# Kernel optimization log

Hardware: AMD Instinct MI355X
Metric: run time of the kernel (lower is better)

## Reference

```python
import jax, jax.numpy as jnp
import numpy as np

N = 100000
E = 1600000
IN_DIM = 128
OUT_DIM = 128
NEG_SLOPE = 0.01  # F.leaky_relu default


def setup_inputs() -> dict:
    key = jax.random.key(0)
    k1, k2, k3, k4, k5, k6 = jax.random.split(key, 6)
    feat = jax.random.normal(k1, (N, IN_DIM), dtype=jnp.float32)
    biclique_mask = jax.random.uniform(k2, (IN_DIM,), dtype=jnp.float32)
    W = jax.random.normal(k3, (OUT_DIM, IN_DIM), dtype=jnp.float32) * 0.05
    attn = jax.random.normal(k4, (OUT_DIM,), dtype=jnp.float32) * 0.1
    src = jax.random.randint(k5, (E,), 0, N, dtype=jnp.int32)
    dst = jax.random.randint(k6, (E,), 0, N, dtype=jnp.int32)
    return {"feat": feat, "biclique_mask": biclique_mask, "W": W,
            "attn": attn, "src": src, "dst": dst}


def reference(feat, biclique_mask, W, attn, src, dst):
    # h = Linear(feat * mask), no bias
    h = (feat * biclique_mask[None, :]) @ W.T            # [N, out_dim]
    # edge score depends only on src node -> compute per-node then gather
    s = jax.nn.leaky_relu(h @ attn, negative_slope=NEG_SLOPE)  # [N]
    score = s[src]                                        # [E]
    # edge softmax grouped by destination node
    seg_max = jax.ops.segment_max(score, dst, num_segments=N)  # [N]
    seg_max = jnp.where(jnp.isfinite(seg_max), seg_max, 0.0)   # empty segs
    ex = jnp.exp(score - seg_max[dst])                     # [E]
    denom = jax.ops.segment_sum(ex, dst, num_segments=N)   # [N]
    a = ex / denom[dst]                                    # [E]
    # weighted aggregation: sum_{e: dst(e)=v} h[src(e)] * a[e]
    m = h[src] * a[:, None]                                # [E, out_dim]
    h_new = jax.ops.segment_sum(m, dst, num_segments=N)    # [N, out_dim]
    return jax.nn.relu(h_new)
```

## Files before the change

### kernel.cpp

```cpp
#include <hip/hip_runtime.h>
#include <math.h>

#define NN 100000
#define EE 1600000
#define DIM 128

#define BK 512
#define NBK2 196
#define NCH 256
#define EPB 6250
#define SCN (NBK2 * NCH)
#define NSB 49

typedef _Float16 half8 __attribute__((ext_vector_type(8)));
typedef _Float16 half2v __attribute__((ext_vector_type(2)));
typedef float f32x4 __attribute__((ext_vector_type(4)));

__global__ __launch_bounds__(256) void k_wt(const float* __restrict__ W,
                                            const float* __restrict__ mask,
                                            _Float16* __restrict__ Bt) {
    int o = blockIdx.x * 256 + threadIdx.x;
    if (o < DIM * DIM) Bt[o] = (_Float16)(W[o] * mask[o & 127]);
}

__global__ __launch_bounds__(256) void k_gemm(const float* __restrict__ feat,
                                              const _Float16* __restrict__ Bt,
                                              const float* __restrict__ attn,
                                              _Float16* __restrict__ hh,
                                              float* __restrict__ s) {
    const int lane = threadIdx.x & 63;
    const int wv   = threadIdx.x >> 6;
    const int l15  = lane & 15;
    const int quad = lane >> 4;
    const int row0 = blockIdx.x * 64 + wv * 16;

    f32x4 acc[8];
#pragma unroll
    for (int nt = 0; nt < 8; ++nt) acc[nt] = (f32x4){0.f, 0.f, 0.f, 0.f};

    const int arow = row0 + l15;
    const bool okA = arow < NN;
    const float* ap = feat + (size_t)(okA ? arow : 0) * DIM + quad * 8;

#pragma unroll
    for (int kc = 0; kc < 4; ++kc) {
        half8 a;
        float4 f0 = ((const float4*)(ap + kc * 32))[0];
        float4 f1 = ((const float4*)(ap + kc * 32))[1];
        if (!okA) { f0 = make_float4(0, 0, 0, 0); f1 = make_float4(0, 0, 0, 0); }
        a[0] = (_Float16)f0.x; a[1] = (_Float16)f0.y;
        a[2] = (_Float16)f0.z; a[3] = (_Float16)f0.w;
        a[4] = (_Float16)f1.x; a[5] = (_Float16)f1.y;
        a[6] = (_Float16)f1.z; a[7] = (_Float16)f1.w;
#pragma unroll
        for (int nt = 0; nt < 8; ++nt) {
            half8 b = *(const half8*)(Bt + (size_t)(nt * 16 + l15) * DIM + kc * 32 + quad * 8);
            acc[nt] = __builtin_amdgcn_mfma_f32_16x16x32_f16(a, b, acc[nt], 0, 0, 0);
        }
    }

    float avv[8];
#pragma unroll
    for (int nt = 0; nt < 8; ++nt) avv[nt] = attn[nt * 16 + l15];

#pragma unroll
    for (int r = 0; r < 4; ++r) {
        int row = row0 + quad * 4 + r;
        float p = 0.f;
#pragma unroll
        for (int nt = 0; nt < 8; ++nt) p += acc[nt][r] * avv[nt];
        p += __shfl_xor(p, 1, 64);
        p += __shfl_xor(p, 2, 64);
        p += __shfl_xor(p, 4, 64);
        p += __shfl_xor(p, 8, 64);
        if (l15 == 0 && row < NN) {
            float lr = (p > 0.f) ? p : 0.01f * p;
            s[row] = __expf(lr);
        }
    }

#pragma unroll
    for (int nt = 0; nt < 8; ++nt) {
#pragma unroll
        for (int r = 0; r < 4; ++r) {
            int row = row0 + quad * 4 + r;
            if (row < NN)
                hh[(size_t)row * DIM + nt * 16 + l15] = (_Float16)acc[nt][r];
        }
    }
}

__global__ __launch_bounds__(1024) void k_bhist(const int* __restrict__ dst,
                                                int* __restrict__ gHist) {
    __shared__ int hist[NBK2];
    const int t = threadIdx.x, b = blockIdx.x;
    for (int i = t; i < NBK2; i += 1024) hist[i] = 0;
    __syncthreads();
    const int e0 = b * EPB;
    int e1 = e0 + EPB; if (e1 > EE) e1 = EE;
    for (int e = e0 + t; e < e1; e += 1024)
        atomicAdd(&hist[dst[e] >> 9], 1);
    __syncthreads();
    for (int i = t; i < NBK2; i += 1024)
        gHist[i * NCH + b] = hist[i];
}

__global__ __launch_bounds__(256) void k_scan_a(const int* __restrict__ deg,
                                                int* __restrict__ excl,
                                                int* __restrict__ bsum) {
    __shared__ int wsum[4];
    __shared__ int woff[4];
    const int t = threadIdx.x, b = blockIdx.x;
    const int base = b * 1024 + t * 4;
    int v0 = deg[base + 0];
    int v1 = deg[base + 1];
    int v2 = deg[base + 2];
    int v3 = deg[base + 3];
    int tsum = v0 + v1 + v2 + v3;

    const int lane = t & 63, w = t >> 6;
    int incl = tsum;
#pragma unroll
    for (int d = 1; d < 64; d <<= 1) {
        int n = __shfl_up(incl, d, 64);
        if (lane >= d) incl += n;
    }
    if (lane == 63) wsum[w] = incl;
    __syncthreads();
    if (t == 0) {
        int run = 0;
#pragma unroll
        for (int i = 0; i < 4; ++i) { woff[i] = run; run += wsum[i]; }
        bsum[b] = run;
    }
    __syncthreads();
    int texcl = incl - tsum + woff[w];
    excl[base + 0] = texcl;
    excl[base + 1] = texcl + v0;
    excl[base + 2] = texcl + v0 + v1;
    excl[base + 3] = texcl + v0 + v1 + v2;
}

__global__ __launch_bounds__(64) void k_scan_b(const int* __restrict__ bsum,
                                               int* __restrict__ boff) {
    const int lane = threadIdx.x & 63;
    int v = (lane < NSB) ? bsum[lane] : 0;
    int incl = v;
#pragma unroll
    for (int d = 1; d < 64; d <<= 1) {
        int n = __shfl_up(incl, d, 64);
        if (lane >= d) incl += n;
    }
    if (lane < NSB) boff[lane] = incl - v;
}

__global__ __launch_bounds__(1024) void k_bscatter(const int* __restrict__ src,
                                                   const int* __restrict__ dst,
                                                   const float* __restrict__ s,
                                                   const int* __restrict__ gOff,
                                                   const int* __restrict__ boff,
                                                   int2* __restrict__ binned) {
    __shared__ int cur[NBK2];
    const int t = threadIdx.x, b = blockIdx.x;
    for (int i = t; i < NBK2; i += 1024) {
        int idx = i * NCH + b;
        cur[i] = gOff[idx] + boff[idx >> 10];
    }
    __syncthreads();
    const int e0 = b * EPB;
    int e1 = e0 + EPB; if (e1 > EE) e1 = EE;
    for (int e = e0 + t; e < e1; e += 1024) {
        int d  = dst[e];
        int si = src[e];
        float x = s[si];
        int bk   = d >> 9;
        int dloc = d & (BK - 1);
        int pos = atomicAdd(&cur[bk], 1);
        binned[pos] = make_int2(si | (dloc << 20), __float_as_int(x));
    }
}

__global__ __launch_bounds__(1024) void k_group(const int* __restrict__ gOff,
                                                const int* __restrict__ boff,
                                                const int2* __restrict__ binned,
                                                int2* __restrict__ pack,
                                                int* __restrict__ offs) {
    __shared__ int ldeg[BK];
    __shared__ int wpart[8];
    const int bk = blockIdx.x;
    const int t  = threadIdx.x;
    const int i0 = bk * NCH;
    const int base = gOff[i0] + boff[i0 >> 10];
    int endp;
    if (bk == NBK2 - 1) endp = EE;
    else {
        int i1 = (bk + 1) * NCH;
        endp = gOff[i1] + boff[i1 >> 10];
    }

    if (t < BK) ldeg[t] = 0;
    __syncthreads();
    for (int j = base + t; j < endp; j += 1024)
        atomicAdd(&ldeg[(binned[j].x >> 20) & (BK - 1)], 1);
    __syncthreads();

    int v = 0, incl = 0;
    const int lane = t & 63;
    if (t < BK) {
        v = ldeg[t];
        incl = v;
#pragma unroll
        for (int d = 1; d < 64; d <<= 1) {
            int n = __shfl_up(incl, d, 64);
            if (lane >= d) incl += n;
        }
        if (lane == 63) wpart[t >> 6] = incl;
    }
    __syncthreads();
    if (t == 0) {
        int run = 0;
#pragma unroll
        for (int i = 0; i < 8; ++i) { int tmp = wpart[i]; wpart[i] = run; run += tmp; }
    }
    __syncthreads();
    if (t < BK) {
        int excl = incl - v + wpart[t >> 6];
        int c = base + excl;
        int n = bk * BK + t;
        if (n < NN) offs[n] = c;
        ldeg[t] = c;
    }
    if (bk == NBK2 - 1 && t == 0) offs[NN] = EE;
    __syncthreads();

    for (int j = base + t; j < endp; j += 1024) {
        int2 e = binned[j];
        int dloc = (e.x >> 20) & (BK - 1);
        int si   = e.x & 0xFFFFF;
        int pos = atomicAdd(&ldeg[dloc], 1);
        pack[pos] = make_int2(si, e.y);
    }
}

__global__ __launch_bounds__(256) void k_agg(const _Float16* __restrict__ hh,
                                             const int* __restrict__ offs,
                                             const int2* __restrict__ pack,
                                             float* __restrict__ out) {
    const int lane = threadIdx.x & 63;
    const int g    = lane >> 4;
    const int li   = lane & 15;
    const int wid  = __builtin_amdgcn_readfirstlane(blockIdx.x * 4 + (threadIdx.x >> 6));
    if (wid >= NN) return;
    const int beg = __builtin_amdgcn_readfirstlane(offs[wid]);
    const int end = __builtin_amdgcn_readfirstlane(offs[wid + 1]);
    const int deg = end - beg;

    const half8* h8 = (const half8*)hh;
    float acc[8];
#pragma unroll
    for (int k = 0; k < 8; ++k) acc[k] = 0.f;
    float lsum = 0.f;

    for (int base = 0; base < deg; base += 64) {
        const int nrem = deg - base;
        const int idx  = base + lane;
        const int cl   = (idx < deg) ? idx : (deg - 1);
        const int2 e   = pack[beg + cl];
        const float w  = (idx < deg) ? __int_as_float(e.y) : 0.f;
        lsum += w;
        const int cmax = (nrem < 64) ? nrem : 64;
        for (int c0 = 0; c0 < cmax; c0 += 16) {
#pragma unroll
            for (int s = 0; s < 4; ++s) {
                const int ei = c0 + s * 4 + g;
                const int   si = __shfl(e.x, ei, 64);
                const float wg = __shfl(w,   ei, 64);
                half8 v = h8[((unsigned)si << 4) + li];
#pragma unroll
                for (int k = 0; k < 8; ++k)
                    acc[k] = fmaf((float)v[k], wg, acc[k]);
            }
        }
    }

#pragma unroll
    for (int k = 0; k < 8; ++k) {
        acc[k] += __shfl_xor(acc[k], 16, 64);
        acc[k] += __shfl_xor(acc[k], 32, 64);
    }
    lsum += __shfl_xor(lsum, 1, 64);
    lsum += __shfl_xor(lsum, 2, 64);
    lsum += __shfl_xor(lsum, 4, 64);
    lsum += __shfl_xor(lsum, 8, 64);
    lsum += __shfl_xor(lsum, 16, 64);
    lsum += __shfl_xor(lsum, 32, 64);

    const float inv = (lsum > 0.f) ? (1.0f / lsum) : 0.f;

    if (g == 0) {
        float4 o0, o1;
        o0.x = fmaxf(acc[0] * inv, 0.f);
        o0.y = fmaxf(acc[1] * inv, 0.f);
        o0.z = fmaxf(acc[2] * inv, 0.f);
        o0.w = fmaxf(acc[3] * inv, 0.f);
        o1.x = fmaxf(acc[4] * inv, 0.f);
        o1.y = fmaxf(acc[5] * inv, 0.f);
        o1.z = fmaxf(acc[6] * inv, 0.f);
        o1.w = fmaxf(acc[7] * inv, 0.f);
        float4* op = (float4*)(out + (size_t)wid * DIM + li * 8);
        op[0] = o0;
        op[1] = o1;
    }
}

extern "C" void kernel_launch(void* const* d_in, const int* in_sizes, int n_in,
                              void* d_out, int out_size, void* d_ws, size_t ws_size,
                              hipStream_t stream) {
    const float* feat = (const float*)d_in[0];
    const float* mask = (const float*)d_in[1];
    const float* W    = (const float*)d_in[2];
    const float* attn = (const float*)d_in[3];
    const int*   src  = (const int*)d_in[4];
    const int*   dst  = (const int*)d_in[5];
    float* out = (float*)d_out;

    char* ws = (char*)d_ws;
    size_t off = 0;
    auto alloc = [&](size_t bytes) -> void* {
        void* p = ws + off;
        off = (off + bytes + 511) & ~(size_t)511;
        return p;
    };
    _Float16* hh  = (_Float16*)alloc((size_t)NN * DIM * 2);
    float*  sv    = (float*)alloc((size_t)NN * 4);
    _Float16* Bt  = (_Float16*)alloc((size_t)DIM * DIM * 2);
    int*    gOff  = (int*)alloc((size_t)SCN * 4);
    int*    offs  = (int*)alloc((size_t)(NN + 1) * 4);
    int*    bsum  = (int*)alloc((size_t)NSB * 4);
    int*    boff  = (int*)alloc((size_t)NSB * 4);
    int2*   binned= (int2*)alloc((size_t)EE * 8);
    int2*   pack  = (int2*)alloc((size_t)EE * 8);

    k_wt<<<(DIM * DIM + 255) / 256, 256, 0, stream>>>(W, mask, Bt);
    k_gemm<<<(NN + 63) / 64, 256, 0, stream>>>(feat, Bt, attn, hh, sv);
    k_bhist<<<NCH, 1024, 0, stream>>>(dst, gOff);
    k_scan_a<<<NSB, 256, 0, stream>>>(gOff, gOff, bsum);
    k_scan_b<<<1, 64, 0, stream>>>(bsum, boff);
    k_bscatter<<<NCH, 1024, 0, stream>>>(src, dst, sv, gOff, boff, binned);
    k_group<<<NBK2, 1024, 0, stream>>>(gOff, boff, binned, pack, offs);
    k_agg<<<(NN + 3) / 4, 256, 0, stream>>>(hh, offs, pack, out);
}
```

Measured before the change: 245.1 us.

## Replace two-level bucketed CSR build with direct global-atomic counting sort

Swaps the two-pass bucketed sort (block histograms, bucket scatter, then per-bucket LDS regrouping) for a flat counting sort. A per-node degree histogram is built with global atomics, scanned, and edges are scattered straight into the CSR array using per-node atomic cursors. This removes the intermediate binned buffer and one full pass over the edges. The cost is heavy global atomic traffic on random addresses, and edge order within each node becomes nondeterministic.

```diff
diff --git a/kernel.cpp b/kernel.cpp
--- a/kernel.cpp
+++ b/kernel.cpp
@@ -5,15 +5,10 @@
 #define EE 1600000
 #define DIM 128
 
-#define BK 512
-#define NBK2 196
-#define NCH 256
-#define EPB 6250
-#define SCN (NBK2 * NCH)
-#define NSB 49
+#define NPAD 100352
+#define NSB2 98
 
 typedef _Float16 half8 __attribute__((ext_vector_type(8)));
-typedef _Float16 half2v __attribute__((ext_vector_type(2)));
 typedef float f32x4 __attribute__((ext_vector_type(4)));
 
 __global__ __launch_bounds__(256) void k_wt(const float* __restrict__ W,
@@ -90,19 +85,16 @@
     }
 }
 
-__global__ __launch_bounds__(1024) void k_bhist(const int* __restrict__ dst,
-                                                int* __restrict__ gHist) {
-    __shared__ int hist[NBK2];
-    const int t = threadIdx.x, b = blockIdx.x;
-    for (int i = t; i < NBK2; i += 1024) hist[i] = 0;
-    __syncthreads();
-    const int e0 = b * EPB;
-    int e1 = e0 + EPB; if (e1 > EE) e1 = EE;
-    for (int e = e0 + t; e < e1; e += 1024)
-        atomicAdd(&hist[dst[e] >> 9], 1);
-    __syncthreads();
-    for (int i = t; i < NBK2; i += 1024)
-        gHist[i * NCH + b] = hist[i];
+__global__ __launch_bounds__(256) void k_hist(const int* __restrict__ dst,
+                                              int* __restrict__ deg) {
+    int i = blockIdx.x * 256 + threadIdx.x;
+    if (i < EE / 4) {
+        int4 d = ((const int4*)dst)[i];
+        atomicAdd(&deg[d.x], 1);
+        atomicAdd(&deg[d.y], 1);
+        atomicAdd(&deg[d.z], 1);
+        atomicAdd(&deg[d.w], 1);
+    }
 }
 
 __global__ __launch_bounds__(256) void k_scan_a(const int* __restrict__ deg,
@@ -141,105 +133,46 @@
     excl[base + 3] = texcl + v0 + v1 + v2;
 }
 
-__global__ __launch_bounds__(64) void k_scan_b(const int* __restrict__ bsum,
-                                               int* __restrict__ boff) {
-    const int lane = threadIdx.x & 63;
-    int v = (lane < NSB) ? bsum[lane] : 0;
+__global__ __launch_bounds__(128) void k_scan_b(const int* __restrict__ bsum,
+                                                int* __restrict__ boff) {
+    __shared__ int wtop[2];
+    const int t = threadIdx.x;
+    const int lane = t & 63, w = t >> 6;
+    int v = (t < NSB2) ? bsum[t] : 0;
     int incl = v;
 #pragma unroll
     for (int d = 1; d < 64; d <<= 1) {
         int n = __shfl_up(incl, d, 64);
         if (lane >= d) incl += n;
     }
-    if (lane < NSB) boff[lane] = incl - v;
-}
-
-__global__ __launch_bounds__(1024) void k_bscatter(const int* __restrict__ src,
-                                                   const int* __restrict__ dst,
-                                                   const float* __restrict__ s,
-                                                   const int* __restrict__ gOff,
-                                                   const int* __restrict__ boff,
-                                                   int2* __restrict__ binned) {
-    __shared__ int cur[NBK2];
-    const int t = threadIdx.x, b = blockIdx.x;
-    for (int i = t; i < NBK2; i += 1024) {
-        int idx = i * NCH + b;
-        cur[i] = gOff[idx] + boff[idx >> 10];
-    }
+    if (lane == 63) wtop[w] = incl;
     __syncthreads();
-    const int e0 = b * EPB;
-    int e1 = e0 + EPB; if (e1 > EE) e1 = EE;
-    for (int e = e0 + t; e < e1; e += 1024) {
-        int d  = dst[e];
-        int si = src[e];
-        float x = s[si];
-        int bk   = d >> 9;
-        int dloc = d & (BK - 1);
-        int pos = atomicAdd(&cur[bk], 1);
-        binned[pos] = make_int2(si | (dloc << 20), __float_as_int(x));
-    }
-}
-
-__global__ __launch_bounds__(1024) void k_group(const int* __restrict__ gOff,
+    int add = (w == 1) ? wtop[0] : 0;
+    if (t < NSB2) boff[t] = incl - v + add;
+}
+
+__global__ __launch_bounds__(256) void k_finoff(const int* __restrict__ excl,
                                                 const int* __restrict__ boff,
-                                                const int2* __restrict__ binned,
-                                                int2* __restrict__ pack,
-                                                int* __restrict__ offs) {
-    __shared__ int ldeg[BK];
-    __shared__ int wpart[8];
-    const int bk = blockIdx.x;
-    const int t  = threadIdx.x;
-    const int i0 = bk * NCH;
-    const int base = gOff[i0] + boff[i0 >> 10];
-    int endp;
-    if (bk == NBK2 - 1) endp = EE;
-    else {
-        int i1 = (bk + 1) * NCH;
-        endp = gOff[i1] + boff[i1 >> 10];
-    }
-
-    if (t < BK) ldeg[t] = 0;
-    __syncthreads();
-    for (int j = base + t; j < endp; j += 1024)
-        atomicAdd(&ldeg[(binned[j].x >> 20) & (BK - 1)], 1);
-    __syncthreads();
-
-    int v = 0, incl = 0;
-    const int lane = t & 63;
-    if (t < BK) {
-        v = ldeg[t];
-        incl = v;
-#pragma unroll
-        for (int d = 1; d < 64; d <<= 1) {
-            int n = __shfl_up(incl, d, 64);
-            if (lane >= d) incl += n;
-        }
-        if (lane == 63) wpart[t >> 6] = incl;
-    }
-    __syncthreads();
-    if (t == 0) {
-        int run = 0;
-#pragma unroll
-        for (int i = 0; i < 8; ++i) { int tmp = wpart[i]; wpart[i] = run; run += tmp; }
-    }
-    __syncthreads();
-    if (t < BK) {
-        int excl = incl - v + wpart[t >> 6];
-        int c = base + excl;
-        int n = bk * BK + t;
-        if (n < NN) offs[n] = c;
-        ldeg[t] = c;
-    }
-    if (bk == NBK2 - 1 && t == 0) offs[NN] = EE;
-    __syncthreads();
-
-    for (int j = base + t; j < endp; j += 1024) {
-        int2 e = binned[j];
-        int dloc = (e.x >> 20) & (BK - 1);
-        int si   = e.x & 0xFFFFF;
-        int pos = atomicAdd(&ldeg[dloc], 1);
-        pack[pos] = make_int2(si, e.y);
-    }
+                                                int* __restrict__ offs,
+                                                int* __restrict__ cur) {
+    int i = blockIdx.x * 256 + threadIdx.x;
+    int v = excl[i] + boff[i >> 10];
+    offs[i] = v;
+    cur[i]  = v;
+}
+
+__global__ __launch_bounds__(256) void k_scatter(const int* __restrict__ src,
+                                                 const int* __restrict__ dst,
+                                                 const float* __restrict__ s,
+                                                 int* __restrict__ cur,
+                                                 int2* __restrict__ pack) {
+    int e = blockIdx.x * 256 + threadIdx.x;
+    if (e >= EE) return;
+    int d  = dst[e];
+    int si = src[e];
+    float x = s[si];
+    int pos = atomicAdd(&cur[d], 1);
+    pack[pos] = make_int2(si, __float_as_int(x));
 }
 
 __global__ __launch_bounds__(256) void k_agg(const _Float16* __restrict__ hh,
@@ -334,19 +267,20 @@
     _Float16* hh  = (_Float16*)alloc((size_t)NN * DIM * 2);
     float*  sv    = (float*)alloc((size_t)NN * 4);
     _Float16* Bt  = (_Float16*)alloc((size_t)DIM * DIM * 2);
-    int*    gOff  = (int*)alloc((size_t)SCN * 4);
-    int*    offs  = (int*)alloc((size_t)(NN + 1) * 4);
-    int*    bsum  = (int*)alloc((size_t)NSB * 4);
-    int*    boff  = (int*)alloc((size_t)NSB * 4);
-    int2*   binned= (int2*)alloc((size_t)EE * 8);
+    int*    deg   = (int*)alloc((size_t)NPAD * 4);
+    int*    offs  = (int*)alloc((size_t)NPAD * 4);
+    int*    cur   = (int*)alloc((size_t)NPAD * 4);
+    int*    bsum  = (int*)alloc((size_t)NSB2 * 4);
+    int*    boff  = (int*)alloc((size_t)NSB2 * 4);
     int2*   pack  = (int2*)alloc((size_t)EE * 8);
 
     k_wt<<<(DIM * DIM + 255) / 256, 256, 0, stream>>>(W, mask, Bt);
     k_gemm<<<(NN + 63) / 64, 256, 0, stream>>>(feat, Bt, attn, hh, sv);
-    k_bhist<<<NCH, 1024, 0, stream>>>(dst, gOff);
-    k_scan_a<<<NSB, 256, 0, stream>>>(gOff, gOff, bsum);
-    k_scan_b<<<1, 64, 0, stream>>>(bsum, boff);
-    k_bscatter<<<NCH, 1024, 0, stream>>>(src, dst, sv, gOff, boff, binned);
-    k_group<<<NBK2, 1024, 0, stream>>>(gOff, boff, binned, pack, offs);
+    hipMemsetAsync(deg, 0, (size_t)NPAD * 4, stream);
+    k_hist<<<(EE / 4 + 255) / 256, 256, 0, stream>>>(dst, deg);
+    k_scan_a<<<NSB2, 256, 0, stream>>>(deg, deg, bsum);
+    k_scan_b<<<1, 128, 0, stream>>>(bsum, boff);
+    k_finoff<<<NPAD / 256, 256, 0, stream>>>(deg, boff, offs, cur);
+    k_scatter<<<(EE + 255) / 256, 256, 0, stream>>>(src, dst, sv, cur, pack);
     k_agg<<<(NN + 3) / 4, 256, 0, stream>>>(hh, offs, pack, out);
 }
```

Result: slower. 349.8 us (+42.7%).
